# Optimization experiments

Hardware: AMD Instinct MI355X
Metric: run time of the kernel (lower is better)

The kernel has to match this reference:

```python
import jax, jax.numpy as jnp
import numpy as np

K = 32
N = 131072


def setup_inputs() -> dict:
    key = jax.random.key(0)
    kx, kmu = jax.random.split(key, 2)
    X = jax.random.normal(kx, (N, 2), dtype=jnp.float32)
    Wk0 = jnp.ones((K,), dtype=jnp.float32) / K
    Wk1k0 = jnp.ones((K, K), dtype=jnp.float32) / K  # column-normalized (sum over axis 0)
    Wk2k1 = jnp.ones((K, K), dtype=jnp.float32) / K
    mu = jax.random.uniform(kmu, (K, K), minval=-4.0, maxval=4.0, dtype=jnp.float32)
    sigma = jnp.full((K, K), 0.5, dtype=jnp.float32)
    return {"X": X, "Wk0": Wk0, "Wk1k0": Wk1k0, "Wk2k1": Wk2k1, "mu": mu, "sigma": sigma}


def _normal_pdf(x, mu, sigma):
    # x: [N]; mu, sigma: [K, K]  ->  [N, K, K]
    z = (x[:, None, None] - mu) / sigma
    inv_sqrt_2pi = 0.3989422804014327
    return jnp.exp(-0.5 * z * z) * (inv_sqrt_2pi / sigma)


def reference(X, Wk0, Wk1k0, Wk2k1, mu, sigma):
    # P0[n, k1, k0] = Normal(mu[k1,k0], sigma[k1,k0]).prob(X[n,0])
    # P1[n, k2, k1] = Normal(mu[k2,k1], sigma[k2,k1]).prob(X[n,1])
    P0 = _normal_pdf(X[:, 0], mu, sigma)
    P1 = _normal_pdf(X[:, 1], mu, sigma)
    # inner[n, k1] = sum_k2 Wk2k1[k2, k1] * P1[n, k2, k1]
    inner = jnp.einsum('nab,ab->nb', P1, Wk2k1)
    # mid[n, k0] = sum_k1 Wk1k0[k1, k0] * P0[n, k1, k0] * inner[n, k1]
    mid = jnp.einsum('nab,ab,na->nb', P0, Wk1k0, inner)
    # likelihood[n] = sum_k0 Wk0[k0] * mid[n, k0]
    likelihoods = mid @ Wk0
    return jnp.log(likelihoods)
```

## Files before the change

kernel.cpp:

```cpp
#include <hip/hip_runtime.h>
#include <hip/hip_bf16.h>
#include <hip/hip_fp16.h>
#include <math.h>

#define KK   32
#define NG   1344
#define NBT  192
#define XLO  (-6.5f)
#define GH   0.01f
#define INVH 100.0f

__device__ __forceinline__ float hw_exp2(float x) {
#if __has_builtin(__builtin_amdgcn_exp2f)
    return __builtin_amdgcn_exp2f(x);
#else
    float r;
    asm("v_exp_f32 %0, %1" : "=v"(r) : "v"(x));
    return r;
#endif
}

__device__ __forceinline__ float hw_log2(float x) {
#if __has_builtin(__builtin_amdgcn_logf)
    return __builtin_amdgcn_logf(x);
#else
    float r;
    asm("v_log_f32 %0, %1" : "=v"(r) : "v"(x));
    return r;
#endif
}

__device__ __forceinline__ unsigned pack_f16(float a, float b) {
    __half2 h = __halves2half2(__float2half_rn(a), __float2half_rn(b));
    return *reinterpret_cast<unsigned*>(&h);
}

__device__ __forceinline__ float2 unpack_f16(unsigned u) {
    __half2 h = *reinterpret_cast<__half2*>(&u);
    return __half22float2(h);
}

__global__ __launch_bounds__(256) void tt_build_grid(
        const float* __restrict__ Wk0,
        const float* __restrict__ Wk1k0,
        const float* __restrict__ Wk2k1,
        const float* __restrict__ mu,
        const float* __restrict__ sigma,
        unsigned* __restrict__ Gp,
        unsigned* __restrict__ Hp) {
    __shared__ float lmu[1056], lA[1056], lC[1056];
    __shared__ float vtmp[8 * 33];
    const int tid    = threadIdx.x;
    const int table  = blockIdx.x >= NBT;
    const int blocal = table ? blockIdx.x - NBT : blockIdx.x;

    const float LOG2E = 1.4426950408889634f;
    const float INV_SQRT_2PI = 0.3989422804014327f;

#pragma unroll
    for (int r = 0; r < 4; ++r) {
        int o = r * 256 + tid;
        int po = (o >> 5) * 33 + (o & 31);
        float inv_s = 1.0f / sigma[o];
        float w = table ? (Wk1k0[o] * Wk0[o & 31]) : Wk2k1[o];
        lmu[po] = mu[o];
        lA[po]  = -0.5f * LOG2E * inv_s * inv_s;
        lC[po]  = w * INV_SQRT_2PI * inv_s;
    }
    __syncthreads();

    const int k1 = tid & 31;
    const int g8 = tid >> 5;
    int i = blocal * 7 + g8;
    if (i > NG - 1) i = NG - 1;
    float x = __builtin_fmaf((float)i, GH, XLO);

    float a0 = 0.0f, a1 = 0.0f, a2 = 0.0f, a3 = 0.0f;
#pragma unroll
    for (int k = 0; k < KK; ++k) {
        int idx = table ? (k1 * 33 + k) : (k * 33 + k1);
        float d = x - lmu[idx];
        float e = hw_exp2(lA[idx] * d * d);
        float t = lC[idx];
        if ((k & 3) == 0)      a0 = __builtin_fmaf(t, e, a0);
        else if ((k & 3) == 1) a1 = __builtin_fmaf(t, e, a1);
        else if ((k & 3) == 2) a2 = __builtin_fmaf(t, e, a2);
        else                   a3 = __builtin_fmaf(t, e, a3);
    }
    float val = hw_log2((a0 + a1) + (a2 + a3));

    vtmp[g8 * 33 + k1] = val;
    __syncthreads();

    if (g8 < 7) {
        int iw = blocal * 7 + g8;
        if (iw <= NG - 2) {
            float vn = vtmp[(g8 + 1) * 33 + k1];
            (table ? Hp : Gp)[iw * KK + k1] = pack_f16(val, vn);
        }
    }
}

__global__ __launch_bounds__(256) void tt_main(const float2* __restrict__ X,
                                               const uint4* __restrict__ G4,
                                               const uint4* __restrict__ H4,
                                               float* __restrict__ out,
                                               int ntot) {
    const int kl8 = threadIdx.x & 7;
    const int grp = (threadIdx.x & 63) >> 3;
    const int gw  = (blockIdx.x * 256 + threadIdx.x) >> 6;
    const int stride = gridDim.x * 32;
    const float LN2 = 0.6931471805599453f;

#pragma unroll 2
    for (int s = gw * 8 + grp; s < ntot; s += stride) {
        float2 x = X[s];

        float u1 = (x.y - XLO) * INVH;
        float u0 = (x.x - XLO) * INVH;
        int i1 = (int)u1; i1 = i1 < 0 ? 0 : (i1 > NG - 2 ? NG - 2 : i1);
        int i0 = (int)u0; i0 = i0 < 0 ? 0 : (i0 > NG - 2 ? NG - 2 : i0);
        float f1 = fminf(fmaxf(u1 - (float)i1, 0.0f), 1.0f);
        float f0 = fminf(fmaxf(u0 - (float)i0, 0.0f), 1.0f);

        uint4 g = G4[i1 * 8 + kl8];
        uint4 h = H4[i0 * 8 + kl8];

        float2 ga = unpack_f16(g.x), gb = unpack_f16(g.y),
               gc = unpack_f16(g.z), gd = unpack_f16(g.w);
        float2 ha = unpack_f16(h.x), hb = unpack_f16(h.y),
               hc = unpack_f16(h.z), hd = unpack_f16(h.w);

        float q0 = __builtin_fmaf(f1, ga.y - ga.x, ga.x)
                 + __builtin_fmaf(f0, ha.y - ha.x, ha.x);
        float q1 = __builtin_fmaf(f1, gb.y - gb.x, gb.x)
                 + __builtin_fmaf(f0, hb.y - hb.x, hb.x);
        float q2 = __builtin_fmaf(f1, gc.y - gc.x, gc.x)
                 + __builtin_fmaf(f0, hc.y - hc.x, hc.x);
        float q3 = __builtin_fmaf(f1, gd.y - gd.x, gd.x)
                 + __builtin_fmaf(f0, hd.y - hd.x, hd.x);
        float e = (hw_exp2(q0) + hw_exp2(q1)) + (hw_exp2(q2) + hw_exp2(q3));

        e += __shfl_xor(e, 1, 8);
        e += __shfl_xor(e, 2, 8);
        e += __shfl_xor(e, 4, 8);

        if (kl8 == 0) out[s] = LN2 * hw_log2(e);
    }
}

extern "C" void kernel_launch(void* const* d_in, const int* in_sizes, int n_in,
                              void* d_out, int out_size, void* d_ws, size_t ws_size,
                              hipStream_t stream) {
    const float* X     = (const float*)d_in[0];
    const float* Wk0   = (const float*)d_in[1];
    const float* Wk1k0 = (const float*)d_in[2];
    const float* Wk2k1 = (const float*)d_in[3];
    const float* mu    = (const float*)d_in[4];
    const float* sigma = (const float*)d_in[5];
    float* out = (float*)d_out;

    unsigned* Gp = (unsigned*)d_ws;
    unsigned* Hp = (unsigned*)((char*)d_ws + (size_t)NG * KK * 4);

    int ntot = in_sizes[0] / 2;

    tt_build_grid<<<2 * NBT, 256, 0, stream>>>(
        Wk0, Wk1k0, Wk2k1, mu, sigma, Gp, Hp);

    tt_main<<<2048, 256, 0, stream>>>(
        (const float2*)X, (const uint4*)Gp, (const uint4*)Hp, out, ntot);
}
```

Baseline: 13.97 us.

## Store interpolation deltas in tables and use 4 lanes per sample without grid-stride loop

The grid builder now stores each table cell as a value plus its difference to the next cell, which removes one subtraction per interpolation in the main kernel. The main kernel assigns 4 lanes per sample, each handling 8 components through two uint4 loads, instead of 8 lanes handling 4 each. This halves the shuffle reduction depth. It also launches one thread group per sample rather than running a fixed 2048-block grid-stride loop. Storing the delta in fp16 may change rounding slightly, and each thread now carries more registers.

```diff
diff --git a/kernel.cpp b/kernel.cpp
--- a/kernel.cpp
+++ b/kernel.cpp
@@ -96,7 +96,7 @@
         int iw = blocal * 7 + g8;
         if (iw <= NG - 2) {
             float vn = vtmp[(g8 + 1) * 33 + k1];
-            (table ? Hp : Gp)[iw * KK + k1] = pack_f16(val, vn);
+            (table ? Hp : Gp)[iw * KK + k1] = pack_f16(val, vn - val);
         }
     }
 }
@@ -106,47 +106,53 @@
                                                const uint4* __restrict__ H4,
                                                float* __restrict__ out,
                                                int ntot) {
-    const int kl8 = threadIdx.x & 7;
-    const int grp = (threadIdx.x & 63) >> 3;
+    const int kl4 = threadIdx.x & 3;
+    const int grp = (threadIdx.x & 63) >> 2;
     const int gw  = (blockIdx.x * 256 + threadIdx.x) >> 6;
-    const int stride = gridDim.x * 32;
+    const int s   = gw * 16 + grp;
+    if (s >= ntot) return;
     const float LN2 = 0.6931471805599453f;
 
-#pragma unroll 2
-    for (int s = gw * 8 + grp; s < ntot; s += stride) {
-        float2 x = X[s];
+    float2 x = X[s];
 
-        float u1 = (x.y - XLO) * INVH;
-        float u0 = (x.x - XLO) * INVH;
-        int i1 = (int)u1; i1 = i1 < 0 ? 0 : (i1 > NG - 2 ? NG - 2 : i1);
-        int i0 = (int)u0; i0 = i0 < 0 ? 0 : (i0 > NG - 2 ? NG - 2 : i0);
-        float f1 = fminf(fmaxf(u1 - (float)i1, 0.0f), 1.0f);
-        float f0 = fminf(fmaxf(u0 - (float)i0, 0.0f), 1.0f);
+    float u1 = (x.y - XLO) * INVH;
+    float u0 = (x.x - XLO) * INVH;
+    int i1 = (int)u1; i1 = i1 < 0 ? 0 : (i1 > NG - 2 ? NG - 2 : i1);
+    int i0 = (int)u0; i0 = i0 < 0 ? 0 : (i0 > NG - 2 ? NG - 2 : i0);
+    float f1 = fminf(fmaxf(u1 - (float)i1, 0.0f), 1.0f);
+    float f0 = fminf(fmaxf(u0 - (float)i0, 0.0f), 1.0f);
 
-        uint4 g = G4[i1 * 8 + kl8];
-        uint4 h = H4[i0 * 8 + kl8];
+    int bg = i1 * 8 + kl4 * 2;
+    int bh = i0 * 8 + kl4 * 2;
+    uint4 ga = G4[bg], gb = G4[bg + 1];
+    uint4 ha = H4[bh], hb = H4[bh + 1];
 
-        float2 ga = unpack_f16(g.x), gb = unpack_f16(g.y),
-               gc = unpack_f16(g.z), gd = unpack_f16(g.w);
-        float2 ha = unpack_f16(h.x), hb = unpack_f16(h.y),
-               hc = unpack_f16(h.z), hd = unpack_f16(h.w);
+    float e = 0.0f;
+    {
+        float2 g0 = unpack_f16(ga.x), h0 = unpack_f16(ha.x);
+        float2 g1 = unpack_f16(ga.y), h1 = unpack_f16(ha.y);
+        float2 g2 = unpack_f16(ga.z), h2 = unpack_f16(ha.z);
+        float2 g3 = unpack_f16(ga.w), h3 = unpack_f16(ha.w);
+        e += hw_exp2(__builtin_fmaf(f1, g0.y, g0.x) + __builtin_fmaf(f0, h0.y, h0.x));
+        e += hw_exp2(__builtin_fmaf(f1, g1.y, g1.x) + __builtin_fmaf(f0, h1.y, h1.x));
+        e += hw_exp2(__builtin_fmaf(f1, g2.y, g2.x) + __builtin_fmaf(f0, h2.y, h2.x));
+        e += hw_exp2(__builtin_fmaf(f1, g3.y, g3.x) + __builtin_fmaf(f0, h3.y, h3.x));
+    }
+    {
+        float2 g0 = unpack_f16(gb.x), h0 = unpack_f16(hb.x);
+        float2 g1 = unpack_f16(gb.y), h1 = unpack_f16(hb.y);
+        float2 g2 = unpack_f16(gb.z), h2 = unpack_f16(hb.z);
+        float2 g3 = unpack_f16(gb.w), h3 = unpack_f16(hb.w);
+        e += hw_exp2(__builtin_fmaf(f1, g0.y, g0.x) + __builtin_fmaf(f0, h0.y, h0.x));
+        e += hw_exp2(__builtin_fmaf(f1, g1.y, g1.x) + __builtin_fmaf(f0, h1.y, h1.x));
+        e += hw_exp2(__builtin_fmaf(f1, g2.y, g2.x) + __builtin_fmaf(f0, h2.y, h2.x));
+        e += hw_exp2(__builtin_fmaf(f1, g3.y, g3.x) + __builtin_fmaf(f0, h3.y, h3.x));
+    }
 
-        float q0 = __builtin_fmaf(f1, ga.y - ga.x, ga.x)
-                 + __builtin_fmaf(f0, ha.y - ha.x, ha.x);
-        float q1 = __builtin_fmaf(f1, gb.y - gb.x, gb.x)
-                 + __builtin_fmaf(f0, hb.y - hb.x, hb.x);
-        float q2 = __builtin_fmaf(f1, gc.y - gc.x, gc.x)
-                 + __builtin_fmaf(f0, hc.y - hc.x, hc.x);
-        float q3 = __builtin_fmaf(f1, gd.y - gd.x, gd.x)
-                 + __builtin_fmaf(f0, hd.y - hd.x, hd.x);
-        float e = (hw_exp2(q0) + hw_exp2(q1)) + (hw_exp2(q2) + hw_exp2(q3));
+    e += __shfl_xor(e, 1, 4);
+    e += __shfl_xor(e, 2, 4);
 
-        e += __shfl_xor(e, 1, 8);
-        e += __shfl_xor(e, 2, 8);
-        e += __shfl_xor(e, 4, 8);
-
-        if (kl8 == 0) out[s] = LN2 * hw_log2(e);
-    }
+    if (kl4 == 0) out[s] = LN2 * hw_log2(e);
 }
 
 extern "C" void kernel_launch(void* const* d_in, const int* in_sizes, int n_in,
@@ -168,6 +174,7 @@
     tt_build_grid<<<2 * NBT, 256, 0, stream>>>(
         Wk0, Wk1k0, Wk2k1, mu, sigma, Gp, Hp);
 
-    tt_main<<<2048, 256, 0, stream>>>(
+    int blocks = (ntot + 63) / 64;
+    tt_main<<<blocks, 256, 0, stream>>>(
         (const float2*)X, (const uint4*)Gp, (const uint4*)Hp, out, ntot);
 }
```

Result: faster. 13.13 us (-6.0%).
